# Kernel tuning notes

Measured on AMD Instinct MI355X. Metric: run time of the kernel, lower is better.

Reference implementation:

```python
import jax, jax.numpy as jnp
import numpy as np

B, T, D = 2, 1024, 2048
E, K, H = 64, 4, 512          # n_experts, top-k, expert_dim
S, HS = 2, H * K              # shared experts, shared hidden dim
CAP = 512


def setup_inputs() -> dict:
    key = jax.random.key(0)
    ks = jax.random.split(key, 9)
    scale = 0.02
    return {
        "x": jax.random.normal(ks[0], (B, T, D), jnp.float32),
        "Wr": jax.random.normal(ks[1], (D, E), jnp.float32) * scale,
        "router_bias": jnp.zeros((E,), jnp.float32),
        "Wg": jax.random.normal(ks[2], (E, D, H), jnp.float32) * scale,
        "Wu": jax.random.normal(ks[3], (E, D, H), jnp.float32) * scale,
        "Wd": jax.random.normal(ks[4], (E, H, D), jnp.float32) * scale,
        "Sg": jax.random.normal(ks[5], (S, D, HS), jnp.float32) * scale,
        "Su": jax.random.normal(ks[6], (S, D, HS), jnp.float32) * scale,
        "Sd": jax.random.normal(ks[7], (S, HS, D), jnp.float32) * scale,
    }


def reference(x, Wr, router_bias, Wg, Wu, Wd, Sg, Su, Sd):
    Bx, Tx, Dx = x.shape
    N = Bx * Tx
    flat = x.reshape(N, Dx)                              # [N, D]

    # ---- router ----
    logits = flat @ Wr + router_bias                     # [N, E]
    scores = jax.nn.softmax(logits, axis=-1)
    topk_scores, topk_idx = jax.lax.top_k(scores, K)     # [N, K]
    topk_scores = topk_scores / topk_scores.sum(-1, keepdims=True)

    eid = topk_idx.reshape(-1)                           # [N*K] expert per assignment
    w = topk_scores.reshape(-1)                          # [N*K] combine weight
    tok = jnp.repeat(jnp.arange(N), K)                   # [N*K] source token id

    # position of each assignment within its expert's buffer
    oh = jax.nn.one_hot(eid, E, dtype=jnp.int32)         # [N*K, E]
    pos = ((jnp.cumsum(oh, axis=0) * oh).sum(-1) - 1)    # [N*K]
    valid = pos < CAP

    # ---- dispatch: scatter tokens into per-expert buffers ----
    xb = jnp.zeros((E, CAP, Dx), x.dtype).at[eid, pos].set(flat[tok], mode="drop")

    # ---- grouped SwiGLU expert FFN ----
    h = jax.nn.silu(jnp.einsum("ecd,edh->ech", xb, Wg)) * jnp.einsum("ecd,edh->ech", xb, Wu)
    yb = jnp.einsum("ech,ehd->ecd", h, Wd)               # [E, CAP, D]

    # ---- combine: gather back and weighted scatter-add to tokens ----
    y = yb[eid, jnp.minimum(pos, CAP - 1)] * (w * valid)[:, None]
    out = jnp.zeros((N, Dx), x.dtype).at[tok].add(y)

    # ---- always-on shared experts ----
    hs = jax.nn.silu(jnp.einsum("nd,sdh->nsh", flat, Sg)) * jnp.einsum("nd,sdh->nsh", flat, Su)
    out = out + jnp.einsum("nsh,shd->nd", hs, Sd)

    return out.reshape(Bx, Tx, Dx)
```

## Files before the change

kernel.cpp:

```cpp
#include <hip/hip_runtime.h>
#include <hip/hip_bf16.h>
#include <stdint.h>

#define N_TOK 2048
#define DM    2048
#define NEXP  64
#define TOPK  4
#define HEXP  512
#define CAPC  512
#define NSH   2
#define HSH   2048
#define RTB   8

typedef __attribute__((ext_vector_type(8))) short short8;
typedef __attribute__((ext_vector_type(4))) float f32x4;
typedef __attribute__((ext_vector_type(4))) float f4;
typedef __attribute__((ext_vector_type(4))) unsigned uint4v;

#define GLDS16(g, l) __builtin_amdgcn_global_load_lds(                     \
    (const __attribute__((address_space(1))) void*)(g),                    \
    (__attribute__((address_space(3))) void*)(l), 16, 0, 0)

#define VMWAIT(N) asm volatile("s_waitcnt vmcnt(" #N ")" ::: "memory")
#define BARX() do { asm volatile("" ::: "memory");                          \
                    __builtin_amdgcn_s_barrier();                           \
                    asm volatile("" ::: "memory"); } while (0)

static __device__ __forceinline__ unsigned short f2bf(float f) {
  union { float f; unsigned u; } v; v.f = f;
  unsigned r = v.u + 0x7FFFu + ((v.u >> 16) & 1u);
  return (unsigned short)(r >> 16);
}

__global__ __launch_bounds__(256) void k_convert(const float* __restrict__ x,
                                                 unsigned short* __restrict__ xb) {
  int i = (blockIdx.x * 256 + threadIdx.x) * 8;
  f4 a = *(const f4*)(x + i);
  f4 b = *(const f4*)(x + i + 4);
  short8 o;
  o[0]=f2bf(a[0]); o[1]=f2bf(a[1]); o[2]=f2bf(a[2]); o[3]=f2bf(a[3]);
  o[4]=f2bf(b[0]); o[5]=f2bf(b[1]); o[6]=f2bf(b[2]); o[7]=f2bf(b[3]);
  *(short8*)(xb + i) = o;
}

#define ARGMAX_ROUND(S,I)                                            \
  { float bv = v; int bi = lane;                                     \
    _Pragma("unroll")                                                \
    for (int o = 32; o; o >>= 1) {                                   \
      float ov = __shfl_xor(bv, o); int oi = __shfl_xor(bi, o);      \
      if (ov > bv || (ov == bv && oi < bi)) { bv = ov; bi = oi; }    \
    }                                                                \
    S = bv; I = bi; if (lane == bi) v = -1.f; }

__global__ __launch_bounds__(256) void k_router(const float* __restrict__ x,
    const float* __restrict__ Wr, const float* __restrict__ bias,
    int* __restrict__ cnt, int* __restrict__ lists, float* __restrict__ wlist) {
  __shared__ float part[4][RTB][64];
  __shared__ float logits[RTB][64];
  int t = threadIdx.x;
  int e = t & 63, sl = t >> 6;
  int tok0 = blockIdx.x * RTB;
  const float* xp = x + (size_t)tok0 * DM;
  float acc[RTB];
#pragma unroll
  for (int i = 0; i < RTB; ++i) acc[i] = 0.f;
  for (int d = sl * 512; d < sl * 512 + 512; ++d) {
    float w = Wr[(size_t)d * NEXP + e];
#pragma unroll
    for (int i = 0; i < RTB; ++i) acc[i] += xp[(size_t)i * DM + d] * w;
  }
#pragma unroll
  for (int i = 0; i < RTB; ++i) part[sl][i][e] = acc[i];
  __syncthreads();
  for (int i = sl; i < RTB; i += 4)
    logits[i][e] = part[0][i][e] + part[1][i][e] + part[2][i][e] + part[3][i][e] + bias[e];
  __syncthreads();
  int lane = t & 63, wv = t >> 6;
  for (int i = wv * 2; i < wv * 2 + 2; ++i) {
    float lg = logits[i][lane];
    float m = lg;
#pragma unroll
    for (int o = 32; o; o >>= 1) m = fmaxf(m, __shfl_xor(m, o));
    float p = expf(lg - m);
    float sm = p;
#pragma unroll
    for (int o = 32; o; o >>= 1) sm += __shfl_xor(sm, o);
    float v = p / sm;
    float s0, s1, s2, s3; int i0, i1, i2, i3;
    ARGMAX_ROUND(s0, i0)
    ARGMAX_ROUND(s1, i1)
    ARGMAX_ROUND(s2, i2)
    ARGMAX_ROUND(s3, i3)
    float tot = s0 + s1 + s2 + s3;
    if (lane < TOPK) {
      float myw = (lane == 0 ? s0 : lane == 1 ? s1 : lane == 2 ? s2 : s3) / tot;
      int   mye = (lane == 0 ? i0 : lane == 1 ? i1 : lane == 2 ? i2 : i3);
      int pos = atomicAdd(&cnt[mye], 1);
      if (pos < CAPC) {
        lists[mye * CAPC + pos] = tok0 + i;
        wlist[mye * CAPC + pos] = myw;
      }
    }
  }
}

__global__ void k_offs(const int* __restrict__ cnt, int* __restrict__ offs) {
  int l = threadIdx.x;
  int c = min(cnt[l], CAPC);
  int sum = c;
#pragma unroll
  for (int o = 1; o < 64; o <<= 1) {
    int ov = __shfl_up(sum, o);
    if (l >= o) sum += ov;
  }
  offs[l + 1] = sum;
  if (l == 0) offs[0] = 0;
}


static __device__ __forceinline__ short8 frag_ldA(const unsigned short* lds, int row, int kElem) {
  int byte = row * 64 + kElem * 2;
  byte ^= ((row >> 1) & 3) << 4;
  return *(const short8*)((const char*)lds + byte);
}

static __device__ __forceinline__ short8 bfragB(const float* lB, int nl, int kb) {
  const float* p = lB + kb * 64 + (nl ^ (((kb >> 3) & 1) << 4));
  float f0 = p[0],   f1 = p[64],  f2 = p[128], f3 = p[192];
  float f4_ = p[256], f5 = p[320], f6 = p[384], f7 = p[448];
  unsigned u0, u1, u2, u3;
  asm("v_cvt_pk_bf16_f32 %0, %1, %2" : "=v"(u0) : "v"(f0),  "v"(f1));
  asm("v_cvt_pk_bf16_f32 %0, %1, %2" : "=v"(u1) : "v"(f2),  "v"(f3));
  asm("v_cvt_pk_bf16_f32 %0, %1, %2" : "=v"(u2) : "v"(f4_), "v"(f5));
  asm("v_cvt_pk_bf16_f32 %0, %1, %2" : "=v"(u3) : "v"(f6),  "v"(f7));
  uint4v uv = {u0, u1, u2, u3};
  return __builtin_bit_cast(short8, uv);
}

static __device__ __forceinline__ void mma1f(const unsigned short* lA, const float* lB,
    f32x4 (&acc)[4][2], int wm, int wn, int lane) {
  int r16 = lane & 15;
  int kb  = (lane >> 4) * 8;
  short8 a[4], b[2];
#pragma unroll
  for (int mf = 0; mf < 4; ++mf) a[mf] = frag_ldA(lA, wm + mf * 16 + r16, kb);
#pragma unroll
  for (int nf = 0; nf < 2; ++nf) b[nf] = bfragB(lB, wn + nf * 16 + r16, kb);
#pragma unroll
  for (int mf = 0; mf < 4; ++mf)
#pragma unroll
    for (int nf = 0; nf < 2; ++nf)
      acc[mf][nf] = __builtin_amdgcn_mfma_f32_16x16x32_bf16(a[mf], b[nf], acc[mf][nf], 0, 0, 0);
}

static __device__ __forceinline__ void mma2f(const unsigned short* lA,
    const float* lBg, const float* lBu,
    f32x4 (&accg)[4][2], f32x4 (&accu)[4][2], int wm, int wn, int lane) {
  int r16 = lane & 15;
  int kb  = (lane >> 4) * 8;
  short8 a[4], bg[2], bu[2];
#pragma unroll
  for (int mf = 0; mf < 4; ++mf) a[mf] = frag_ldA(lA, wm + mf * 16 + r16, kb);
#pragma unroll
  for (int nf = 0; nf < 2; ++nf) {
    bg[nf] = bfragB(lBg, wn + nf * 16 + r16, kb);
    bu[nf] = bfragB(lBu, wn + nf * 16 + r16, kb);
  }
#pragma unroll
  for (int mf = 0; mf < 4; ++mf)
#pragma unroll
    for (int nf = 0; nf < 2; ++nf) {
      accg[mf][nf] = __builtin_amdgcn_mfma_f32_16x16x32_bf16(a[mf], bg[nf], accg[mf][nf], 0, 0, 0);
      accu[mf][nf] = __builtin_amdgcn_mfma_f32_16x16x32_bf16(a[mf], bu[nf], accu[mf][nf], 0, 0, 0);
    }
}

static __device__ __forceinline__ float silu_mul(float g, float u) {
  return g / (1.f + expf(-g)) * u;
}

#define A_SETUP(asrc, SROW_EXPR)                                            \
  const unsigned short* asrc[2];                                            \
  {                                                                         \
    _Pragma("unroll")                                                       \
    for (int p = 0; p < 2; ++p) {                                           \
      int row = p * 64 + wv * 16 + (lane >> 2);                             \
      int srow = (SROW_EXPR);                                               \
      asrc[p] = Abase + (size_t)srow * lda                                  \
              + (((lane & 3) ^ ((row >> 1) & 3)) << 3);                     \
    }                                                                       \
  }
#define A_STAGE(asrc, lAbuf, k0)                                            \
  { _Pragma("unroll")                                                       \
    for (int p = 0; p < 2; ++p)                                             \
      GLDS16(asrc[p] + (k0), (lAbuf) + p * 2048 + wv * 512); }

#define B_SETUP(bsrc, Bbase, ldb)                                           \
  const float* bsrc[2];                                                     \
  {                                                                         \
    _Pragma("unroll")                                                       \
    for (int p = 0; p < 2; ++p) {                                           \
      int k = p * 16 + wv * 4 + (lane >> 4);                                \
      int c = (lane & 15) ^ (((k >> 3) & 1) << 2);                          \
      bsrc[p] = (Bbase) + (size_t)k * (ldb) + n0 + c * 4;                   \
    }                                                                       \
  }
#define B_STAGE(bsrc, lBbuf, k0, ldb)                                       \
  { _Pragma("unroll")                                                       \
    for (int p = 0; p < 2; ++p)                                             \
      GLDS16(bsrc[p] + (size_t)(k0) * (ldb), (lBbuf) + p * 1024 + wv * 256); }

__global__ __launch_bounds__(256, 3) void k_expert_gateup(const unsigned short* __restrict__ xbf,
    const float* __restrict__ Wg, const float* __restrict__ Wu,
    const int* __restrict__ cnt, const int* __restrict__ offs,
    const int* __restrict__ lists, unsigned short* __restrict__ hws) {
  int e = blockIdx.y;
  int ne = min(cnt[e], CAPC);
  if (ne == 0) return;
  int n0 = blockIdx.x * 64;
  const float* Bg = Wg + (size_t)e * DM * HEXP;
  const float* Bu = Wu + (size_t)e * DM * HEXP;
  const int* lst = lists + e * CAPC;
  int base = offs[e];
  __shared__ unsigned short lA[2][128 * 32];
  __shared__ float lBg[2][32 * 64];
  __shared__ float lBu[2][32 * 64];
  int tid = threadIdx.x;
  int lane = tid & 63, wv = tid >> 6;
  int wm = (wv >> 1) * 64, wn = (wv & 1) * 32;
  const unsigned short* Abase = xbf; const int lda = DM;
  B_SETUP(bgsrc, Bg, HEXP)
  B_SETUP(busrc, Bu, HEXP)
  const int NT = DM / 32;
  for (int m0 = 0; m0 < ne; m0 += 128) {
    A_SETUP(asrc, lst[min(m0 + row, ne - 1)])
    f32x4 accg[4][2] = {};
    f32x4 accu[4][2] = {};
    A_STAGE(asrc, lA[0], 0)  B_STAGE(bgsrc, lBg[0], 0, HEXP)  B_STAGE(busrc, lBu[0], 0, HEXP)
    A_STAGE(asrc, lA[1], 32) B_STAGE(bgsrc, lBg[1], 32, HEXP) B_STAGE(busrc, lBu[1], 32, HEXP)
    VMWAIT(6); BARX();
#pragma unroll 1
    for (int t = 0; t < NT; t += 2) {
      mma2f(lA[0], lBg[0], lBu[0], accg, accu, wm, wn, lane);
      BARX();
      if (t + 2 < NT) {
        int k2 = (t + 2) * 32;
        A_STAGE(asrc, lA[0], k2) B_STAGE(bgsrc, lBg[0], k2, HEXP) B_STAGE(busrc, lBu[0], k2, HEXP)
        VMWAIT(6);
      } else { VMWAIT(0); }
      BARX();
      mma2f(lA[1], lBg[1], lBu[1], accg, accu, wm, wn, lane);
      if (t + 2 < NT) {
        BARX();
        if (t + 3 < NT) {
          int k3 = (t + 3) * 32;
          A_STAGE(asrc, lA[1], k3) B_STAGE(bgsrc, lBg[1], k3, HEXP) B_STAGE(busrc, lBu[1], k3, HEXP)
          VMWAIT(6);
        } else { VMWAIT(0); }
        BARX();
      }
    }
    BARX();
#pragma unroll
    for (int mf = 0; mf < 4; ++mf)
#pragma unroll
      for (int r = 0; r < 4; ++r) {
        int rl = m0 + wm + mf * 16 + (lane >> 4) * 4 + r;
        if (rl < ne) {
#pragma unroll
          for (int nf = 0; nf < 2; ++nf) {
            int col = n0 + wn + nf * 16 + (lane & 15);
            float h = silu_mul(accg[mf][nf][r], accu[mf][nf][r]);
            hws[(size_t)(base + rl) * HEXP + col] = f2bf(h);
          }
        }
      }
  }
}

__global__ __launch_bounds__(256, 3) void k_shared_gateup(const unsigned short* __restrict__ xbf,
    const float* __restrict__ Sg, const float* __restrict__ Su,
    unsigned short* __restrict__ hs) {
  int n0 = blockIdx.x * 64;
  int m0 = blockIdx.y * 128;
  int s  = blockIdx.z;
  const float* Bg = Sg + (size_t)s * DM * HSH;
  const float* Bu = Su + (size_t)s * DM * HSH;
  __shared__ unsigned short lA[2][128 * 32];
  __shared__ float lBg[2][32 * 64];
  __shared__ float lBu[2][32 * 64];
  int tid = threadIdx.x;
  int lane = tid & 63, wv = tid >> 6;
  int wm = (wv >> 1) * 64, wn = (wv & 1) * 32;
  const unsigned short* Abase = xbf; const int lda = DM;
  B_SETUP(bgsrc, Bg, HSH)
  B_SETUP(busrc, Bu, HSH)
  A_SETUP(asrc, m0 + row)
  f32x4 accg[4][2] = {};
  f32x4 accu[4][2] = {};
  const int NT = DM / 32;
  A_STAGE(asrc, lA[0], 0)  B_STAGE(bgsrc, lBg[0], 0, HSH)  B_STAGE(busrc, lBu[0], 0, HSH)
  A_STAGE(asrc, lA[1], 32) B_STAGE(bgsrc, lBg[1], 32, HSH) B_STAGE(busrc, lBu[1], 32, HSH)
  VMWAIT(6); BARX();
#pragma unroll 1
  for (int t = 0; t < NT; t += 2) {
    mma2f(lA[0], lBg[0], lBu[0], accg, accu, wm, wn, lane);
    BARX();
    if (t + 2 < NT) {
      int k2 = (t + 2) * 32;
      A_STAGE(asrc, lA[0], k2) B_STAGE(bgsrc, lBg[0], k2, HSH) B_STAGE(busrc, lBu[0], k2, HSH)
      VMWAIT(6);
    } else { VMWAIT(0); }
    BARX();
    mma2f(lA[1], lBg[1], lBu[1], accg, accu, wm, wn, lane);
    if (t + 2 < NT) {
      BARX();
      if (t + 3 < NT) {
        int k3 = (t + 3) * 32;
        A_STAGE(asrc, lA[1], k3) B_STAGE(bgsrc, lBg[1], k3, HSH) B_STAGE(busrc, lBu[1], k3, HSH)
        VMWAIT(6);
      } else { VMWAIT(0); }
      BARX();
    }
  }
#pragma unroll
  for (int mf = 0; mf < 4; ++mf)
#pragma unroll
    for (int nf = 0; nf < 2; ++nf)
#pragma unroll
      for (int r = 0; r < 4; ++r) {
        int row = m0 + wm + mf * 16 + (lane >> 4) * 4 + r;
        int col = n0 + wn + nf * 16 + (lane & 15);
        float h = silu_mul(accg[mf][nf][r], accu[mf][nf][r]);
        hs[(size_t)row * (NSH * HSH) + s * HSH + col] = f2bf(h);
      }
}

__global__ __launch_bounds__(256, 4) void k_shared_down(const unsigned short* __restrict__ hs,
    const float* __restrict__ Sd, float* __restrict__ out) {
  int n0 = blockIdx.x * 64;
  int m0 = blockIdx.y * 128;
  __shared__ unsigned short lA[2][128 * 32];
  __shared__ float lB[2][32 * 64];
  int tid = threadIdx.x;
  int lane = tid & 63, wv = tid >> 6;
  int wm = (wv >> 1) * 64, wn = (wv & 1) * 32;
  const unsigned short* Abase = hs; const int lda = NSH * HSH;
  B_SETUP(bsrc, Sd, DM)
  A_SETUP(asrc, m0 + row)
  f32x4 acc[4][2] = {};
  const int NT = (NSH * HSH) / 32;
  A_STAGE(asrc, lA[0], 0)  B_STAGE(bsrc, lB[0], 0, DM)
  A_STAGE(asrc, lA[1], 32) B_STAGE(bsrc, lB[1], 32, DM)
  VMWAIT(4); BARX();
#pragma unroll 1
  for (int t = 0; t < NT; t += 2) {
    mma1f(lA[0], lB[0], acc, wm, wn, lane);
    BARX();
    if (t + 2 < NT) {
      int k2 = (t + 2) * 32;
      A_STAGE(asrc, lA[0], k2) B_STAGE(bsrc, lB[0], k2, DM)
      VMWAIT(4);
    } else { VMWAIT(0); }
    BARX();
    mma1f(lA[1], lB[1], acc, wm, wn, lane);
    if (t + 2 < NT) {
      BARX();
      if (t + 3 < NT) {
        int k3 = (t + 3) * 32;
        A_STAGE(asrc, lA[1], k3) B_STAGE(bsrc, lB[1], k3, DM)
        VMWAIT(4);
      } else { VMWAIT(0); }
      BARX();
    }
  }
#pragma unroll
  for (int mf = 0; mf < 4; ++mf)
#pragma unroll
    for (int nf = 0; nf < 2; ++nf)
#pragma unroll
      for (int r = 0; r < 4; ++r) {
        int row = m0 + wm + mf * 16 + (lane >> 4) * 4 + r;
        int col = n0 + wn + nf * 16 + (lane & 15);
        out[(size_t)row * DM + col] = acc[mf][nf][r];
      }
}

__global__ __launch_bounds__(256, 4) void k_expert_down(const unsigned short* __restrict__ hws,
    const float* __restrict__ Wd, const int* __restrict__ cnt, const int* __restrict__ offs,
    const int* __restrict__ lists, const float* __restrict__ wlist,
    float* __restrict__ out) {
  int e = blockIdx.y;
  int ne = min(cnt[e], CAPC);
  if (ne == 0) return;
  int n0 = blockIdx.x * 64;
  const float* B = Wd + (size_t)e * HEXP * DM;
  __shared__ unsigned short lA[2][128 * 32];
  __shared__ float lB[2][32 * 64];
  int tid = threadIdx.x;
  int lane = tid & 63, wv = tid >> 6;
  int wm = (wv >> 1) * 64, wn = (wv & 1) * 32;
  const unsigned short* Abase = hws + (size_t)offs[e] * HEXP; const int lda = HEXP;
  B_SETUP(bsrc, B, DM)
  const int NT = HEXP / 32;
  for (int m0 = 0; m0 < ne; m0 += 128) {
    A_SETUP(asrc, min(m0 + row, ne - 1))
    f32x4 acc[4][2] = {};
    A_STAGE(asrc, lA[0], 0)  B_STAGE(bsrc, lB[0], 0, DM)
    A_STAGE(asrc, lA[1], 32) B_STAGE(bsrc, lB[1], 32, DM)
    VMWAIT(4); BARX();
#pragma unroll 1
    for (int t = 0; t < NT; t += 2) {
      mma1f(lA[0], lB[0], acc, wm, wn, lane);
      BARX();
      if (t + 2 < NT) {
        int k2 = (t + 2) * 32;
        A_STAGE(asrc, lA[0], k2) B_STAGE(bsrc, lB[0], k2, DM)
        VMWAIT(4);
      } else { VMWAIT(0); }
      BARX();
      mma1f(lA[1], lB[1], acc, wm, wn, lane);
      if (t + 2 < NT) {
        BARX();
        if (t + 3 < NT) {
          int k3 = (t + 3) * 32;
          A_STAGE(asrc, lA[1], k3) B_STAGE(bsrc, lB[1], k3, DM)
          VMWAIT(4);
        } else { VMWAIT(0); }
        BARX();
      }
    }
    BARX();
#pragma unroll
    for (int mf = 0; mf < 4; ++mf)
#pragma unroll
      for (int r = 0; r < 4; ++r) {
        int rl = m0 + wm + mf * 16 + (lane >> 4) * 4 + r;
        if (rl < ne) {
          int tok  = lists[e * CAPC + rl];
          float w  = wlist[e * CAPC + rl];
#pragma unroll
          for (int nf = 0; nf < 2; ++nf) {
            int col = n0 + wn + nf * 16 + (lane & 15);
            atomicAdd(out + (size_t)tok * DM + col, acc[mf][nf][r] * w);
          }
        }
      }
  }
}

extern "C" void kernel_launch(void* const* d_in, const int* in_sizes, int n_in,
                              void* d_out, int out_size, void* d_ws, size_t ws_size,
                              hipStream_t stream) {
  const float* x    = (const float*)d_in[0];
  const float* Wr   = (const float*)d_in[1];
  const float* bias = (const float*)d_in[2];
  const float* Wg   = (const float*)d_in[3];
  const float* Wu   = (const float*)d_in[4];
  const float* Wd   = (const float*)d_in[5];
  const float* Sg   = (const float*)d_in[6];
  const float* Su   = (const float*)d_in[7];
  const float* Sd   = (const float*)d_in[8];
  float* out = (float*)d_out;
  char* ws = (char*)d_ws;

  const size_t off_cnt   = 0;
  const size_t off_offs  = 256;
  const size_t off_lists = 1024;
  const size_t off_wlist = off_lists + (size_t)NEXP * CAPC * 4;
  const size_t off_xbf   = off_wlist + (size_t)NEXP * CAPC * 4;
  const size_t off_hs    = off_xbf + (size_t)N_TOK * DM * 2;
  const size_t off_h     = off_hs + (size_t)N_TOK * NSH * HSH * 2;
  const size_t req       = off_h + (size_t)N_TOK * TOPK * HEXP * 2;
  if (ws_size < req) return;

  int* cnt            = (int*)(ws + off_cnt);
  int* offs           = (int*)(ws + off_offs);
  int* lists          = (int*)(ws + off_lists);
  float* wlist        = (float*)(ws + off_wlist);
  unsigned short* xbf = (unsigned short*)(ws + off_xbf);
  unsigned short* hs  = (unsigned short*)(ws + off_hs);
  unsigned short* hws = (unsigned short*)(ws + off_h);

  hipMemsetAsync(cnt, 0, NEXP * sizeof(int), stream);
  k_convert<<<(N_TOK * DM) / (256 * 8), 256, 0, stream>>>(x, xbf);
  k_router<<<N_TOK / RTB, 256, 0, stream>>>(x, Wr, bias, cnt, lists, wlist);
  k_offs<<<1, 64, 0, stream>>>(cnt, offs);
  k_expert_gateup<<<dim3(HEXP / 64, NEXP), 256, 0, stream>>>(xbf, Wg, Wu, cnt, offs, lists, hws);
  k_shared_gateup<<<dim3(HSH / 64, N_TOK / 128, NSH), 256, 0, stream>>>(xbf, Sg, Su, hs);
  k_shared_down<<<dim3(DM / 64, N_TOK / 128), 256, 0, stream>>>(hs, Sd, out);
  k_expert_down<<<dim3(DM / 64, NEXP), 256, 0, stream>>>(hws, Wd, cnt, offs, lists, wlist, out);
}
```

Measured before the change: 662.5 us.

## Prepack fp32 weights into blocked bf16 layout before the expert and shared GEMMs

Adds a k_wblock pass that converts every fp32 weight matrix (expert gate/up/down and shared gate/up/down) into bf16 k-pair-interleaved, column-blocked, swizzled blobs in the workspace on each call. New GEMM kernels then stream contiguous bf16 tiles into LDS and build MFMA B fragments from four 32-bit LDS reads, with no per-fragment conversion. This is meant to cut LDS traffic and conversion work in the inner loops, especially in the shared GEMMs where each weight tile is reused across many token tiles. The cost is an extra full read of all weights plus a bf16 write every call, and the blocked path only runs when the workspace is large enough; otherwise the renamed original kernels are used.

```diff
diff --git a/kernel.cpp b/kernel.cpp
--- a/kernel.cpp
+++ b/kernel.cpp
@@ -30,6 +30,12 @@
   union { float f; unsigned u; } v; v.f = f;
   unsigned r = v.u + 0x7FFFu + ((v.u >> 16) & 1u);
   return (unsigned short)(r >> 16);
+}
+
+static __device__ __forceinline__ unsigned pk2(float lo, float hi) {
+  unsigned u;
+  asm("v_cvt_pk_bf16_f32 %0, %1, %2" : "=v"(u) : "v"(lo), "v"(hi));
+  return u;
 }
 
 __global__ __launch_bounds__(256) void k_convert(const float* __restrict__ x,
@@ -117,62 +123,10 @@
   if (l == 0) offs[0] = 0;
 }
 
-
 static __device__ __forceinline__ short8 frag_ldA(const unsigned short* lds, int row, int kElem) {
   int byte = row * 64 + kElem * 2;
   byte ^= ((row >> 1) & 3) << 4;
   return *(const short8*)((const char*)lds + byte);
-}
-
-static __device__ __forceinline__ short8 bfragB(const float* lB, int nl, int kb) {
-  const float* p = lB + kb * 64 + (nl ^ (((kb >> 3) & 1) << 4));
-  float f0 = p[0],   f1 = p[64],  f2 = p[128], f3 = p[192];
-  float f4_ = p[256], f5 = p[320], f6 = p[384], f7 = p[448];
-  unsigned u0, u1, u2, u3;
-  asm("v_cvt_pk_bf16_f32 %0, %1, %2" : "=v"(u0) : "v"(f0),  "v"(f1));
-  asm("v_cvt_pk_bf16_f32 %0, %1, %2" : "=v"(u1) : "v"(f2),  "v"(f3));
-  asm("v_cvt_pk_bf16_f32 %0, %1, %2" : "=v"(u2) : "v"(f4_), "v"(f5));
-  asm("v_cvt_pk_bf16_f32 %0, %1, %2" : "=v"(u3) : "v"(f6),  "v"(f7));
-  uint4v uv = {u0, u1, u2, u3};
-  return __builtin_bit_cast(short8, uv);
-}
-
-static __device__ __forceinline__ void mma1f(const unsigned short* lA, const float* lB,
-    f32x4 (&acc)[4][2], int wm, int wn, int lane) {
-  int r16 = lane & 15;
-  int kb  = (lane >> 4) * 8;
-  short8 a[4], b[2];
-#pragma unroll
-  for (int mf = 0; mf < 4; ++mf) a[mf] = frag_ldA(lA, wm + mf * 16 + r16, kb);
-#pragma unroll
-  for (int nf = 0; nf < 2; ++nf) b[nf] = bfragB(lB, wn + nf * 16 + r16, kb);
-#pragma unroll
-  for (int mf = 0; mf < 4; ++mf)
-#pragma unroll
-    for (int nf = 0; nf < 2; ++nf)
-      acc[mf][nf] = __builtin_amdgcn_mfma_f32_16x16x32_bf16(a[mf], b[nf], acc[mf][nf], 0, 0, 0);
-}
-
-static __device__ __forceinline__ void mma2f(const unsigned short* lA,
-    const float* lBg, const float* lBu,
-    f32x4 (&accg)[4][2], f32x4 (&accu)[4][2], int wm, int wn, int lane) {
-  int r16 = lane & 15;
-  int kb  = (lane >> 4) * 8;
-  short8 a[4], bg[2], bu[2];
-#pragma unroll
-  for (int mf = 0; mf < 4; ++mf) a[mf] = frag_ldA(lA, wm + mf * 16 + r16, kb);
-#pragma unroll
-  for (int nf = 0; nf < 2; ++nf) {
-    bg[nf] = bfragB(lBg, wn + nf * 16 + r16, kb);
-    bu[nf] = bfragB(lBu, wn + nf * 16 + r16, kb);
-  }
-#pragma unroll
-  for (int mf = 0; mf < 4; ++mf)
-#pragma unroll
-    for (int nf = 0; nf < 2; ++nf) {
-      accg[mf][nf] = __builtin_amdgcn_mfma_f32_16x16x32_bf16(a[mf], bg[nf], accg[mf][nf], 0, 0, 0);
-      accu[mf][nf] = __builtin_amdgcn_mfma_f32_16x16x32_bf16(a[mf], bu[nf], accu[mf][nf], 0, 0, 0);
-    }
 }
 
 static __device__ __forceinline__ float silu_mul(float g, float u) {
@@ -195,6 +149,356 @@
     for (int p = 0; p < 2; ++p)                                             \
       GLDS16(asrc[p] + (k0), (lAbuf) + p * 2048 + wv * 512); }
 
+
+__global__ __launch_bounds__(256) void k_wblock(const float* __restrict__ src,
+    unsigned* __restrict__ dst, int K2, int N, int k2chunks) {
+  int m   = blockIdx.x / k2chunks;
+  int k2c = blockIdx.x % k2chunks;
+  int t = threadIdx.x;
+  int k2 = k2c * 8 + (t >> 5);
+  int nbCount = N >> 6;
+  const float* s0 = src + ((size_t)m * 2 * K2 + 2 * k2) * N;
+  const float* s1 = s0 + N;
+  unsigned* dbase = dst + (size_t)m * nbCount * K2 * 64;
+  int x = ((k2 >> 2) & 3) << 4;
+  for (int sB = (t & 31) * 8; sB < N; sB += 256) {
+    int nb = sB >> 6;
+    int n8 = (nb << 6) + ((sB & 63) ^ x);
+    f4 a0 = *(const f4*)(s0 + n8); f4 a1 = *(const f4*)(s0 + n8 + 4);
+    f4 b0 = *(const f4*)(s1 + n8); f4 b1 = *(const f4*)(s1 + n8 + 4);
+    uint4v v0 = { pk2(a0[0], b0[0]), pk2(a0[1], b0[1]), pk2(a0[2], b0[2]), pk2(a0[3], b0[3]) };
+    uint4v v1 = { pk2(a1[0], b1[0]), pk2(a1[1], b1[1]), pk2(a1[2], b1[2]), pk2(a1[3], b1[3]) };
+    unsigned* d = dbase + ((size_t)nb * K2 + k2) * 64 + (sB & 63);
+    *(uint4v*)d = v0;
+    *(uint4v*)(d + 4) = v1;
+  }
+}
+
+static __device__ __forceinline__ short8 bfragBlk(const unsigned* lB, int n, int kq) {
+  uint4v v;
+#pragma unroll
+  for (int i = 0; i < 4; ++i) {
+    int k2 = kq + i;
+    v[i] = lB[k2 * 64 + (n ^ (((k2 >> 2) & 3) << 4))];
+  }
+  return __builtin_bit_cast(short8, v);
+}
+
+static __device__ __forceinline__ void mma2blk(const unsigned short* lA,
+    const unsigned* lBg, const unsigned* lBu,
+    f32x4 (&accg)[4][2], f32x4 (&accu)[4][2], int wm, int wn, int lane) {
+  int r16 = lane & 15, kb = (lane >> 4) * 8, kq = (lane >> 4) * 4;
+  short8 a[4], bg[2], bu[2];
+#pragma unroll
+  for (int mf = 0; mf < 4; ++mf) a[mf] = frag_ldA(lA, wm + mf * 16 + r16, kb);
+#pragma unroll
+  for (int nf = 0; nf < 2; ++nf) {
+    int n = wn + nf * 16 + r16;
+    bg[nf] = bfragBlk(lBg, n, kq);
+    bu[nf] = bfragBlk(lBu, n, kq);
+  }
+#pragma unroll
+  for (int mf = 0; mf < 4; ++mf)
+#pragma unroll
+    for (int nf = 0; nf < 2; ++nf) {
+      accg[mf][nf] = __builtin_amdgcn_mfma_f32_16x16x32_bf16(a[mf], bg[nf], accg[mf][nf], 0, 0, 0);
+      accu[mf][nf] = __builtin_amdgcn_mfma_f32_16x16x32_bf16(a[mf], bu[nf], accu[mf][nf], 0, 0, 0);
+    }
+}
+
+static __device__ __forceinline__ void mma1blk(const unsigned short* lA, const unsigned* lB,
+    f32x4 (&acc)[4][2], int wm, int wn, int lane) {
+  int r16 = lane & 15, kb = (lane >> 4) * 8, kq = (lane >> 4) * 4;
+  short8 a[4], b[2];
+#pragma unroll
+  for (int mf = 0; mf < 4; ++mf) a[mf] = frag_ldA(lA, wm + mf * 16 + r16, kb);
+#pragma unroll
+  for (int nf = 0; nf < 2; ++nf) b[nf] = bfragBlk(lB, wn + nf * 16 + r16, kq);
+#pragma unroll
+  for (int mf = 0; mf < 4; ++mf)
+#pragma unroll
+    for (int nf = 0; nf < 2; ++nf)
+      acc[mf][nf] = __builtin_amdgcn_mfma_f32_16x16x32_bf16(a[mf], b[nf], acc[mf][nf], 0, 0, 0);
+}
+
+__global__ __launch_bounds__(256, 2) void k_gu_blk(const unsigned short* __restrict__ xbf,
+    const unsigned* __restrict__ gblob, const unsigned* __restrict__ ublob,
+    const int* __restrict__ cnt, const int* __restrict__ offs,
+    const int* __restrict__ lists, unsigned short* __restrict__ hws) {
+  int bid = blockIdx.x;
+  int e = bid >> 3, nb = bid & 7, n0 = nb * 64;
+  int ne = min(cnt[e], CAPC);
+  if (ne == 0) return;
+  const int* lst = lists + e * CAPC;
+  int base = offs[e];
+  __shared__ unsigned short lA[2][128 * 32];
+  __shared__ unsigned lBg[2][16 * 64];
+  __shared__ unsigned lBu[2][16 * 64];
+  int tid = threadIdx.x, lane = tid & 63, wv = tid >> 6;
+  int wm = (wv >> 1) * 64, wn = (wv & 1) * 32;
+  const unsigned short* Abase = xbf; const int lda = DM;
+  const unsigned* bg = gblob + (size_t)(e * 8 + nb) * 1024 * 64 + wv * 256 + lane * 4;
+  const unsigned* bu = ublob + (size_t)(e * 8 + nb) * 1024 * 64 + wv * 256 + lane * 4;
+  const int NT = 64;
+  for (int m0 = 0; m0 < ne; m0 += 128) {
+    A_SETUP(asrc, lst[min(m0 + row, ne - 1)])
+    f32x4 accg[4][2] = {}; f32x4 accu[4][2] = {};
+    A_STAGE(asrc, lA[0], 0)  GLDS16(bg, lBg[0] + wv * 256); GLDS16(bu, lBu[0] + wv * 256);
+    A_STAGE(asrc, lA[1], 32) GLDS16(bg + 1024, lBg[1] + wv * 256); GLDS16(bu + 1024, lBu[1] + wv * 256);
+    VMWAIT(4); BARX();
+#pragma unroll 1
+    for (int t = 0; t < NT; t += 2) {
+      mma2blk(lA[0], lBg[0], lBu[0], accg, accu, wm, wn, lane);
+      BARX();
+      if (t + 2 < NT) {
+        A_STAGE(asrc, lA[0], (t + 2) * 32)
+        GLDS16(bg + (size_t)(t + 2) * 1024, lBg[0] + wv * 256);
+        GLDS16(bu + (size_t)(t + 2) * 1024, lBu[0] + wv * 256);
+        VMWAIT(4);
+      } else { VMWAIT(0); }
+      BARX();
+      mma2blk(lA[1], lBg[1], lBu[1], accg, accu, wm, wn, lane);
+      if (t + 2 < NT) {
+        BARX();
+        if (t + 3 < NT) {
+          A_STAGE(asrc, lA[1], (t + 3) * 32)
+          GLDS16(bg + (size_t)(t + 3) * 1024, lBg[1] + wv * 256);
+          GLDS16(bu + (size_t)(t + 3) * 1024, lBu[1] + wv * 256);
+          VMWAIT(4);
+        } else { VMWAIT(0); }
+        BARX();
+      }
+    }
+    BARX();
+#pragma unroll
+    for (int mf = 0; mf < 4; ++mf)
+#pragma unroll
+      for (int r = 0; r < 4; ++r) {
+        int rl = m0 + wm + mf * 16 + (lane >> 4) * 4 + r;
+        if (rl < ne) {
+#pragma unroll
+          for (int nf = 0; nf < 2; ++nf) {
+            int col = n0 + wn + nf * 16 + (lane & 15);
+            float h = silu_mul(accg[mf][nf][r], accu[mf][nf][r]);
+            hws[(size_t)(base + rl) * HEXP + col] = f2bf(h);
+          }
+        }
+      }
+  }
+}
+
+__global__ __launch_bounds__(256, 2) void k_down_blk(const unsigned short* __restrict__ hws,
+    const unsigned* __restrict__ dblob, const int* __restrict__ cnt, const int* __restrict__ offs,
+    const int* __restrict__ lists, const float* __restrict__ wlist, float* __restrict__ out) {
+  int bid = blockIdx.x;
+  int e = bid >> 5, nb = bid & 31, n0 = nb * 64;
+  int ne = min(cnt[e], CAPC);
+  if (ne == 0) return;
+  __shared__ unsigned short lA[2][128 * 32];
+  __shared__ unsigned lB[2][16 * 64];
+  int tid = threadIdx.x, lane = tid & 63, wv = tid >> 6;
+  int wm = (wv >> 1) * 64, wn = (wv & 1) * 32;
+  const unsigned short* Abase = hws + (size_t)offs[e] * HEXP; const int lda = HEXP;
+  const unsigned* bb = dblob + (size_t)(e * 32 + nb) * 256 * 64 + wv * 256 + lane * 4;
+  const int NT = 16;
+  for (int m0 = 0; m0 < ne; m0 += 128) {
+    A_SETUP(asrc, min(m0 + row, ne - 1))
+    f32x4 acc[4][2] = {};
+    A_STAGE(asrc, lA[0], 0)  GLDS16(bb, lB[0] + wv * 256);
+    A_STAGE(asrc, lA[1], 32) GLDS16(bb + 1024, lB[1] + wv * 256);
+    VMWAIT(3); BARX();
+#pragma unroll 1
+    for (int t = 0; t < NT; t += 2) {
+      mma1blk(lA[0], lB[0], acc, wm, wn, lane);
+      BARX();
+      if (t + 2 < NT) {
+        A_STAGE(asrc, lA[0], (t + 2) * 32)
+        GLDS16(bb + (size_t)(t + 2) * 1024, lB[0] + wv * 256);
+        VMWAIT(3);
+      } else { VMWAIT(0); }
+      BARX();
+      mma1blk(lA[1], lB[1], acc, wm, wn, lane);
+      if (t + 2 < NT) {
+        BARX();
+        if (t + 3 < NT) {
+          A_STAGE(asrc, lA[1], (t + 3) * 32)
+          GLDS16(bb + (size_t)(t + 3) * 1024, lB[1] + wv * 256);
+          VMWAIT(3);
+        } else { VMWAIT(0); }
+        BARX();
+      }
+    }
+    BARX();
+#pragma unroll
+    for (int mf = 0; mf < 4; ++mf)
+#pragma unroll
+      for (int r = 0; r < 4; ++r) {
+        int rl = m0 + wm + mf * 16 + (lane >> 4) * 4 + r;
+        if (rl < ne) {
+          int tok = lists[e * CAPC + rl];
+          float w = wlist[e * CAPC + rl];
+#pragma unroll
+          for (int nf = 0; nf < 2; ++nf) {
+            int col = n0 + wn + nf * 16 + (lane & 15);
+            atomicAdd(out + (size_t)tok * DM + col, acc[mf][nf][r] * w);
+          }
+        }
+      }
+  }
+}
+
+__global__ __launch_bounds__(256, 2) void k_sgu_blk(const unsigned short* __restrict__ xbf,
+    const unsigned* __restrict__ sgblob, const unsigned* __restrict__ sublob,
+    unsigned short* __restrict__ hs) {
+  int bid = blockIdx.x;
+  int s = bid >> 9, mb = (bid >> 5) & 15, nb = bid & 31;
+  int m0 = mb * 128, n0 = nb * 64;
+  __shared__ unsigned short lA[2][128 * 32];
+  __shared__ unsigned lBg[2][16 * 64];
+  __shared__ unsigned lBu[2][16 * 64];
+  int tid = threadIdx.x, lane = tid & 63, wv = tid >> 6;
+  int wm = (wv >> 1) * 64, wn = (wv & 1) * 32;
+  const unsigned short* Abase = xbf; const int lda = DM;
+  const unsigned* bg = sgblob + (size_t)(s * 32 + nb) * 1024 * 64 + wv * 256 + lane * 4;
+  const unsigned* bu = sublob + (size_t)(s * 32 + nb) * 1024 * 64 + wv * 256 + lane * 4;
+  const int NT = 64;
+  A_SETUP(asrc, m0 + row)
+  f32x4 accg[4][2] = {}; f32x4 accu[4][2] = {};
+  A_STAGE(asrc, lA[0], 0)  GLDS16(bg, lBg[0] + wv * 256); GLDS16(bu, lBu[0] + wv * 256);
+  A_STAGE(asrc, lA[1], 32) GLDS16(bg + 1024, lBg[1] + wv * 256); GLDS16(bu + 1024, lBu[1] + wv * 256);
+  VMWAIT(4); BARX();
+#pragma unroll 1
+  for (int t = 0; t < NT; t += 2) {
+    mma2blk(lA[0], lBg[0], lBu[0], accg, accu, wm, wn, lane);
+    BARX();
+    if (t + 2 < NT) {
+      A_STAGE(asrc, lA[0], (t + 2) * 32)
+      GLDS16(bg + (size_t)(t + 2) * 1024, lBg[0] + wv * 256);
+      GLDS16(bu + (size_t)(t + 2) * 1024, lBu[0] + wv * 256);
+      VMWAIT(4);
+    } else { VMWAIT(0); }
+    BARX();
+    mma2blk(lA[1], lBg[1], lBu[1], accg, accu, wm, wn, lane);
+    if (t + 2 < NT) {
+      BARX();
+      if (t + 3 < NT) {
+        A_STAGE(asrc, lA[1], (t + 3) * 32)
+        GLDS16(bg + (size_t)(t + 3) * 1024, lBg[1] + wv * 256);
+        GLDS16(bu + (size_t)(t + 3) * 1024, lBu[1] + wv * 256);
+        VMWAIT(4);
+      } else { VMWAIT(0); }
+      BARX();
+    }
+  }
+#pragma unroll
+  for (int mf = 0; mf < 4; ++mf)
+#pragma unroll
+    for (int nf = 0; nf < 2; ++nf)
+#pragma unroll
+      for (int r = 0; r < 4; ++r) {
+        int row = m0 + wm + mf * 16 + (lane >> 4) * 4 + r;
+        int col = n0 + wn + nf * 16 + (lane & 15);
+        float h = silu_mul(accg[mf][nf][r], accu[mf][nf][r]);
+        hs[(size_t)row * (NSH * HSH) + s * HSH + col] = f2bf(h);
+      }
+}
+
+__global__ __launch_bounds__(256, 2) void k_sd_blk(const unsigned short* __restrict__ hs,
+    const unsigned* __restrict__ sdblob, float* __restrict__ out) {
+  int bid = blockIdx.x;
+  int mb = bid >> 5, nb = bid & 31;
+  int m0 = mb * 128, n0 = nb * 64;
+  __shared__ unsigned short lA[2][128 * 32];
+  __shared__ unsigned lB[2][16 * 64];
+  int tid = threadIdx.x, lane = tid & 63, wv = tid >> 6;
+  int wm = (wv >> 1) * 64, wn = (wv & 1) * 32;
+  const unsigned short* Abase = hs; const int lda = NSH * HSH;
+  const unsigned* bb = sdblob + (size_t)nb * 2048 * 64 + wv * 256 + lane * 4;
+  const int NT = 128;
+  A_SETUP(asrc, m0 + row)
+  f32x4 acc[4][2] = {};
+  A_STAGE(asrc, lA[0], 0)  GLDS16(bb, lB[0] + wv * 256);
+  A_STAGE(asrc, lA[1], 32) GLDS16(bb + 1024, lB[1] + wv * 256);
+  VMWAIT(3); BARX();
+#pragma unroll 1
+  for (int t = 0; t < NT; t += 2) {
+    mma1blk(lA[0], lB[0], acc, wm, wn, lane);
+    BARX();
+    if (t + 2 < NT) {
+      A_STAGE(asrc, lA[0], (t + 2) * 32)
+      GLDS16(bb + (size_t)(t + 2) * 1024, lB[0] + wv * 256);
+      VMWAIT(3);
+    } else { VMWAIT(0); }
+    BARX();
+    mma1blk(lA[1], lB[1], acc, wm, wn, lane);
+    if (t + 2 < NT) {
+      BARX();
+      if (t + 3 < NT) {
+        A_STAGE(asrc, lA[1], (t + 3) * 32)
+        GLDS16(bb + (size_t)(t + 3) * 1024, lB[1] + wv * 256);
+        VMWAIT(3);
+      } else { VMWAIT(0); }
+      BARX();
+    }
+  }
+#pragma unroll
+  for (int mf = 0; mf < 4; ++mf)
+#pragma unroll
+    for (int nf = 0; nf < 2; ++nf)
+#pragma unroll
+      for (int r = 0; r < 4; ++r) {
+        int row = m0 + wm + mf * 16 + (lane >> 4) * 4 + r;
+        int col = n0 + wn + nf * 16 + (lane & 15);
+        out[(size_t)row * DM + col] = acc[mf][nf][r];
+      }
+}
+
+static __device__ __forceinline__ short8 bfragB(const float* lB, int nl, int kb) {
+  const float* p = lB + kb * 64 + (nl ^ (((kb >> 3) & 1) << 4));
+  float f0 = p[0],   f1 = p[64],  f2 = p[128], f3 = p[192];
+  float f4_ = p[256], f5 = p[320], f6 = p[384], f7 = p[448];
+  uint4v uv = { pk2(f0, f1), pk2(f2, f3), pk2(f4_, f5), pk2(f6, f7) };
+  return __builtin_bit_cast(short8, uv);
+}
+
+static __device__ __forceinline__ void mma1f(const unsigned short* lA, const float* lB,
+    f32x4 (&acc)[4][2], int wm, int wn, int lane) {
+  int r16 = lane & 15;
+  int kb  = (lane >> 4) * 8;
+  short8 a[4], b[2];
+#pragma unroll
+  for (int mf = 0; mf < 4; ++mf) a[mf] = frag_ldA(lA, wm + mf * 16 + r16, kb);
+#pragma unroll
+  for (int nf = 0; nf < 2; ++nf) b[nf] = bfragB(lB, wn + nf * 16 + r16, kb);
+#pragma unroll
+  for (int mf = 0; mf < 4; ++mf)
+#pragma unroll
+    for (int nf = 0; nf < 2; ++nf)
+      acc[mf][nf] = __builtin_amdgcn_mfma_f32_16x16x32_bf16(a[mf], b[nf], acc[mf][nf], 0, 0, 0);
+}
+
+static __device__ __forceinline__ void mma2f(const unsigned short* lA,
+    const float* lBg, const float* lBu,
+    f32x4 (&accg)[4][2], f32x4 (&accu)[4][2], int wm, int wn, int lane) {
+  int r16 = lane & 15;
+  int kb  = (lane >> 4) * 8;
+  short8 a[4], bg[2], bu[2];
+#pragma unroll
+  for (int mf = 0; mf < 4; ++mf) a[mf] = frag_ldA(lA, wm + mf * 16 + r16, kb);
+#pragma unroll
+  for (int nf = 0; nf < 2; ++nf) {
+    bg[nf] = bfragB(lBg, wn + nf * 16 + r16, kb);
+    bu[nf] = bfragB(lBu, wn + nf * 16 + r16, kb);
+  }
+#pragma unroll
+  for (int mf = 0; mf < 4; ++mf)
+#pragma unroll
+    for (int nf = 0; nf < 2; ++nf) {
+      accg[mf][nf] = __builtin_amdgcn_mfma_f32_16x16x32_bf16(a[mf], bg[nf], accg[mf][nf], 0, 0, 0);
+      accu[mf][nf] = __builtin_amdgcn_mfma_f32_16x16x32_bf16(a[mf], bu[nf], accu[mf][nf], 0, 0, 0);
+    }
+}
+
 #define B_SETUP(bsrc, Bbase, ldb)                                           \
   const float* bsrc[2];                                                     \
   {                                                                         \
@@ -210,7 +514,7 @@
     for (int p = 0; p < 2; ++p)                                             \
       GLDS16(bsrc[p] + (size_t)(k0) * (ldb), (lBbuf) + p * 1024 + wv * 256); }
 
-__global__ __launch_bounds__(256, 3) void k_expert_gateup(const unsigned short* __restrict__ xbf,
+__global__ __launch_bounds__(256, 3) void k_gu_fb(const unsigned short* __restrict__ xbf,
     const float* __restrict__ Wg, const float* __restrict__ Wu,
     const int* __restrict__ cnt, const int* __restrict__ offs,
     const int* __restrict__ lists, unsigned short* __restrict__ hws) {
@@ -225,8 +529,7 @@
   __shared__ unsigned short lA[2][128 * 32];
   __shared__ float lBg[2][32 * 64];
   __shared__ float lBu[2][32 * 64];
-  int tid = threadIdx.x;
-  int lane = tid & 63, wv = tid >> 6;
+  int tid = threadIdx.x, lane = tid & 63, wv = tid >> 6;
   int wm = (wv >> 1) * 64, wn = (wv & 1) * 32;
   const unsigned short* Abase = xbf; const int lda = DM;
   B_SETUP(bgsrc, Bg, HEXP)
@@ -278,7 +581,7 @@
   }
 }
 
-__global__ __launch_bounds__(256, 3) void k_shared_gateup(const unsigned short* __restrict__ xbf,
+__global__ __launch_bounds__(256, 3) void k_sgu_fb(const unsigned short* __restrict__ xbf,
     const float* __restrict__ Sg, const float* __restrict__ Su,
     unsigned short* __restrict__ hs) {
   int n0 = blockIdx.x * 64;
@@ -289,8 +592,7 @@
   __shared__ unsigned short lA[2][128 * 32];
   __shared__ float lBg[2][32 * 64];
   __shared__ float lBu[2][32 * 64];
-  int tid = threadIdx.x;
-  int lane = tid & 63, wv = tid >> 6;
+  int tid = threadIdx.x, lane = tid & 63, wv = tid >> 6;
   int wm = (wv >> 1) * 64, wn = (wv & 1) * 32;
   const unsigned short* Abase = xbf; const int lda = DM;
   B_SETUP(bgsrc, Bg, HSH)
@@ -336,14 +638,13 @@
       }
 }
 
-__global__ __launch_bounds__(256, 4) void k_shared_down(const unsigned short* __restrict__ hs,
+__global__ __launch_bounds__(256, 4) void k_sd_fb(const unsigned short* __restrict__ hs,
     const float* __restrict__ Sd, float* __restrict__ out) {
   int n0 = blockIdx.x * 64;
   int m0 = blockIdx.y * 128;
   __shared__ unsigned short lA[2][128 * 32];
   __shared__ float lB[2][32 * 64];
-  int tid = threadIdx.x;
-  int lane = tid & 63, wv = tid >> 6;
+  int tid = threadIdx.x, lane = tid & 63, wv = tid >> 6;
   int wm = (wv >> 1) * 64, wn = (wv & 1) * 32;
   const unsigned short* Abase = hs; const int lda = NSH * HSH;
   B_SETUP(bsrc, Sd, DM)
@@ -386,7 +687,7 @@
       }
 }
 
-__global__ __launch_bounds__(256, 4) void k_expert_down(const unsigned short* __restrict__ hws,
+__global__ __launch_bounds__(256, 4) void k_down_fb(const unsigned short* __restrict__ hws,
     const float* __restrict__ Wd, const int* __restrict__ cnt, const int* __restrict__ offs,
     const int* __restrict__ lists, const float* __restrict__ wlist,
     float* __restrict__ out) {
@@ -397,8 +698,7 @@
   const float* B = Wd + (size_t)e * HEXP * DM;
   __shared__ unsigned short lA[2][128 * 32];
   __shared__ float lB[2][32 * 64];
-  int tid = threadIdx.x;
-  int lane = tid & 63, wv = tid >> 6;
+  int tid = threadIdx.x, lane = tid & 63, wv = tid >> 6;
   int wm = (wv >> 1) * 64, wn = (wv & 1) * 32;
   const unsigned short* Abase = hws + (size_t)offs[e] * HEXP; const int lda = HEXP;
   B_SETUP(bsrc, B, DM)
@@ -471,8 +771,18 @@
   const size_t off_xbf   = off_wlist + (size_t)NEXP * CAPC * 4;
   const size_t off_hs    = off_xbf + (size_t)N_TOK * DM * 2;
   const size_t off_h     = off_hs + (size_t)N_TOK * NSH * HSH * 2;
-  const size_t req       = off_h + (size_t)N_TOK * TOPK * HEXP * 2;
-  if (ws_size < req) return;
+  const size_t off_blob  = (off_h + (size_t)N_TOK * TOPK * HEXP * 2 + 255) & ~(size_t)255;
+  const size_t GB = (size_t)64 * 8 * 1024 * 64 * 4;
+  const size_t SB = (size_t)64 * 1024 * 64 * 4;
+  const size_t off_g  = off_blob;
+  const size_t off_u  = off_g + GB;
+  const size_t off_d  = off_u + GB;
+  const size_t off_sg = off_d + GB;
+  const size_t off_su = off_sg + SB;
+  const size_t off_sd = off_su + SB;
+  const size_t req_blk = off_sd + SB;
+  const size_t req_fb  = off_blob;
+  if (ws_size < req_fb) return;
 
   int* cnt            = (int*)(ws + off_cnt);
   int* offs           = (int*)(ws + off_offs);
@@ -486,8 +796,28 @@
   k_convert<<<(N_TOK * DM) / (256 * 8), 256, 0, stream>>>(x, xbf);
   k_router<<<N_TOK / RTB, 256, 0, stream>>>(x, Wr, bias, cnt, lists, wlist);
   k_offs<<<1, 64, 0, stream>>>(cnt, offs);
-  k_expert_gateup<<<dim3(HEXP / 64, NEXP), 256, 0, stream>>>(xbf, Wg, Wu, cnt, offs, lists, hws);
-  k_shared_gateup<<<dim3(HSH / 64, N_TOK / 128, NSH), 256, 0, stream>>>(xbf, Sg, Su, hs);
-  k_shared_down<<<dim3(DM / 64, N_TOK / 128), 256, 0, stream>>>(hs, Sd, out);
-  k_expert_down<<<dim3(DM / 64, NEXP), 256, 0, stream>>>(hws, Wd, cnt, offs, lists, wlist, out);
-}
+
+  if (ws_size >= req_blk) {
+    unsigned* gblob  = (unsigned*)(ws + off_g);
+    unsigned* ublob  = (unsigned*)(ws + off_u);
+    unsigned* dblob  = (unsigned*)(ws + off_d);
+    unsigned* sgblob = (unsigned*)(ws + off_sg);
+    unsigned* sublob = (unsigned*)(ws + off_su);
+    unsigned* sdblob = (unsigned*)(ws + off_sd);
+    k_wblock<<<64 * 128, 256, 0, stream>>>(Wg, gblob, 1024, 512, 128);
+    k_wblock<<<64 * 128, 256, 0, stream>>>(Wu, ublob, 1024, 512, 128);
+    k_wblock<<<64 * 32, 256, 0, stream>>>(Wd, dblob, 256, 2048, 32);
+    k_wblock<<<2 * 128, 256, 0, stream>>>(Sg, sgblob, 1024, 2048, 128);
+    k_wblock<<<2 * 128, 256, 0, stream>>>(Su, sublob, 1024, 2048, 128);
+    k_wblock<<<256, 256, 0, stream>>>(Sd, sdblob, 2048, 2048, 256);
+    k_gu_blk<<<512, 256, 0, stream>>>(xbf, gblob, ublob, cnt, offs, lists, hws);
+    k_sgu_blk<<<1024, 256, 0, stream>>>(xbf, sgblob, sublob, hs);
+    k_sd_blk<<<512, 256, 0, stream>>>(hs, sdblob, out);
+    k_down_blk<<<2048, 256, 0, stream>>>(hws, dblob, cnt, offs, lists, wlist, out);
+  } else {
+    k_gu_fb<<<dim3(HEXP / 64, NEXP), 256, 0, stream>>>(xbf, Wg, Wu, cnt, offs, lists, hws);
+    k_sgu_fb<<<dim3(HSH / 64, N_TOK / 128, NSH), 256, 0, stream>>>(xbf, Sg, Su, hs);
+    k_sd_fb<<<dim3(DM / 64, N_TOK / 128), 256, 0, stream>>>(hs, Sd, out);
+    k_down_fb<<<dim3(DM / 64, NEXP), 256, 0, stream>>>(hws, Wd, cnt, offs, lists, wlist, out);
+  }
+}
```

Result: slower. 771.9 us (+16.5%).
